# Kernel optimization log

Measured on AMD Instinct MI355X. Metric: run time of the kernel, lower is better.

Reference implementation:

```python
import jax, jax.numpy as jnp
import numpy as np

NN_SIZE = 10  # matches init_kwargs nn_size


def _knn_idx(points, k):
    """points: (B,N,D). Returns (B,N,k) indices of k nearest neighbors, self excluded."""
    sq = jnp.sum(points * points, axis=-1)  # (B,N)
    # squared euclidean distances (B,N,N)
    d2 = sq[:, :, None] + sq[:, None, :] - 2.0 * jnp.einsum('bnd,bmd->bnm', points, points)
    _, idx = jax.lax.top_k(-d2, k + 1)  # smallest distances; first hit is self
    return idx[:, :, 1:]  # drop self -> (B,N,k)


def _uniform_laplacian(points, knn_idx):
    """points: (B,N,D); knn_idx: (B,N,K). lap = mean(neighbors) - point."""
    neigh = jax.vmap(lambda p, i: p[i])(points, knn_idx)  # (B,N,K,D) gather per batch
    return jnp.mean(neigh, axis=2) - points


def setup_inputs() -> dict:
    key = jax.random.key(0)
    k1, k2 = jax.random.split(key)
    B, N, D = 2, 8192, 3
    point1 = jax.random.normal(k1, (B, N, D), dtype=jnp.float32)
    point2 = jax.random.normal(k2, (B, N, D), dtype=jnp.float32)
    return {"point1": point1, "point2": point2}


def reference(point1, point2):
    knn_idx = _knn_idx(point1, NN_SIZE)          # connectivity from ref cloud
    lap1 = _uniform_laplacian(point1, knn_idx)   # (B,N,3)
    lap2 = _uniform_laplacian(point2, knn_idx)   # reuse knn_idx
    # metric = L1Loss (mean reduction); use_norm=False
    return jnp.mean(jnp.abs(lap1 - lap2))
```

## Files before the change

kernel.cpp:

```cpp
#include <hip/hip_runtime.h>
#include <math.h>


constexpr int NPTS  = 8192;
constexpr int NB    = 2;
constexpr int KNN   = 10;
constexpr int QPB   = 64;
constexpr int WPB   = 16;
constexpr int P1BLOCK = 256;
constexpr int P1GRID  = NB * NPTS / (P1BLOCK / WPB);
constexpr int MASK13 = 0xFFFFE000;

constexpr int   G    = 32;
constexpr int   NC   = G * G * G;
constexpr float BMIN = -5.5f;
constexpr float BW   = 11.0f;
constexpr float H    = BW / G;
constexpr float INVH = (float)G / BW;

__device__ __forceinline__ void ins1(int l[KNN], int x) {
#pragma unroll
    for (int k = KNN - 1; k > 0; --k) l[k] = min(l[k], max(l[k - 1], x));
    l[0] = min(l[0], x);
}
__device__ __forceinline__ void ins2(int l[KNN], int a, int b) {
    const int b0 = min(a, b), b1 = max(a, b);
#pragma unroll
    for (int k = KNN - 1; k >= 2; --k)
        l[k] = min(l[k], min(max(l[k - 1], b0), max(l[k - 2], b1)));
    l[1] = min(l[1], min(max(l[0], b0), b1));
    l[0] = min(l[0], b0);
}
template<int S>
__device__ __forceinline__ void ins2s(int l[KNN], int a, int b) {
    const int b0 = min(a, b), b1 = max(a, b);
#pragma unroll
    for (int k = KNN - 1; k >= S + 2; --k)
        l[k] = min(l[k], min(max(l[k - 1], b0), max(l[k - 2], b1)));
    l[S + 1] = min(l[S + 1], min(max(l[S], b0), b1));
    l[S] = min(l[S], b0);
}
__device__ __forceinline__ void merge_sorted(int l[KNN], const int p[KNN]) {
    ins2s<0>(l, p[0], p[1]);
    ins2s<2>(l, p[2], p[3]);
    ins2s<4>(l, p[4], p[5]);
    ins2s<6>(l, p[6], p[7]);
    ins2s<8>(l, p[8], p[9]);
}

__global__ void pack_bin(const float* __restrict__ p1, float4* __restrict__ w,
                         int* __restrict__ hist, int* __restrict__ cellof,
                         float* __restrict__ out, int* __restrict__ nfail) {
    const int i = blockIdx.x * blockDim.x + threadIdx.x;
    if (i >= NB * NPTS) return;
    if (i == 0) { out[0] = 0.0f; nfail[0] = 0; }
    const float x = p1[3 * i], y = p1[3 * i + 1], z = p1[3 * i + 2];
    w[i] = make_float4(x, y, z, fmaf(x, x, fmaf(y, y, z * z)));
    const int cx = min(max((int)floorf((x - BMIN) * INVH), 0), G - 1);
    const int cy = min(max((int)floorf((y - BMIN) * INVH), 0), G - 1);
    const int cz = min(max((int)floorf((z - BMIN) * INVH), 0), G - 1);
    const int c = (cz << 10) | (cy << 5) | cx;
    cellof[i] = c;
    atomicAdd(&hist[(i >> 13) * NC + c], 1);
}

__global__ __launch_bounds__(1024)
void scan_cells(const int* __restrict__ hist, int* __restrict__ starts) {
    __shared__ int wsum[16];
    const int b = blockIdx.x, t = threadIdx.x;
    const int* hb = hist + b * NC;
    int* sb = starts + b * (NC + 1);
    const int c0 = t * 32;
    const int4* hb4 = (const int4*)(hb + c0);
    int loc[32]; int sum = 0;
#pragma unroll
    for (int j = 0; j < 8; ++j) {
        const int4 v = hb4[j];
        loc[4 * j + 0] = v.x; loc[4 * j + 1] = v.y;
        loc[4 * j + 2] = v.z; loc[4 * j + 3] = v.w;
        sum += v.x + v.y + v.z + v.w;
    }
    const int lane = t & 63, wvi = t >> 6;
    int incl = sum;
#pragma unroll
    for (int off = 1; off < 64; off <<= 1) {
        const int v = __shfl_up(incl, off);
        if (lane >= off) incl += v;
    }
    if (lane == 63) wsum[wvi] = incl;
    __syncthreads();
    if (t < 16) {
        const int v = wsum[t];
        int iv = v;
#pragma unroll
        for (int off = 1; off < 16; off <<= 1) {
            const int u = __shfl_up(iv, off);
            if (t >= off) iv += u;
        }
        wsum[t] = iv - v;
    }
    __syncthreads();
    int run = wsum[wvi] + incl - sum;
#pragma unroll
    for (int j = 0; j < 32; ++j) { sb[c0 + j] = run; run += loc[j]; }
    if (t == 1023) sb[NC] = run;
}

__global__ void scatter_all(const int* __restrict__ cellof,
                            const int* __restrict__ starts,
                            int* __restrict__ hist,
                            const float4* __restrict__ w,
                            const float* __restrict__ p2,
                            float4* __restrict__ wsorted,
                            float4* __restrict__ p2s) {
    const int i = blockIdx.x * blockDim.x + threadIdx.x;
    if (i >= NB * NPTS) return;
    const int b = i >> 13;
    const int c = cellof[i];
    const int old = atomicSub(&hist[b * NC + c], 1);
    const int pos = b * NPTS + starts[b * (NC + 1) + c] + old - 1;
    wsorted[pos] = w[i];
    p2s[pos] = make_float4(p2[3 * i], p2[3 * i + 1], p2[3 * i + 2], 0.0f);
}

template<int S>
__device__ __forceinline__ void scan_batched(const float4* __restrict__ W,
                                             const int* __restrict__ st,
                                             int cx, int cy, int cz,
                                             float m2x, float m2y, float m2z,
                                             float q2, int qpos, int sl,
                                             int l[KNN])
{
    constexpr int Wd = 2 * S + 1;
    constexpr int R  = Wd * Wd;
    constexpr int CH = 5;
    const int IMAX = 0x7FFFFFFF;
    int J0[R], J1[R];
#pragma unroll
    for (int r = 0; r < R; ++r) {
        const int dy = r % Wd - S, dz = r / Wd - S;
        const int ay = cy + dy, az = cz + dz;
        const bool ok = ((unsigned)ay < G) && ((unsigned)az < G);
        const int cbase = (az << 10) | (ay << 5);
        const int lo = cbase + max(cx - S, 0);
        const int hi = cbase + min(cx + S, G - 1) + 1;
        J0[r] = ok ? st[lo] : 0;
        J1[r] = ok ? st[hi] : 0;
    }
#pragma unroll
    for (int base = 0; base < R; base += CH) {
        float4 P[CH];
#pragma unroll
        for (int c = 0; c < CH; ++c) {
            const int r = base + c;
            if (r < R) {
                const int j = min(J0[r] + sl, NPTS - 1);
                P[c] = W[j];
            }
        }
#pragma unroll
        for (int c = 0; c < CH; ++c) {
            const int r = base + c;
            if (r < R) {
                const int j1 = J1[r];
                int j = J0[r] + sl;
                if (j < j1) {
                    float4 c4 = P[c];
                    while (true) {
                        const int jn = j + WPB;
                        const bool more = jn < j1;
                        float4 nx;
                        if (more) nx = W[jn];
                        const float d2 = fmaf(m2x, c4.x,
                                         fmaf(m2y, c4.y,
                                         fmaf(m2z, c4.z, c4.w + q2)));
                        int key = (__float_as_int(d2) & MASK13) | j;
                        key = (j == qpos) ? IMAX : key;
                        ins1(l, key);
                        if (!more) break;
                        c4 = nx; j = jn;
                    }
                }
            }
        }
    }
}

__global__ __launch_bounds__(P1BLOCK)
void phase1(const float4* __restrict__ wsorted, const float4* __restrict__ p2s,
            const int* __restrict__ starts, float* __restrict__ out,
            int* __restrict__ nfail, int* __restrict__ worklist)
{
    __shared__ float red[P1BLOCK / 64];

    const int tid = threadIdx.x;
    const int sl  = tid & 15;
    const int gw  = (tid >> 4) & 3;
    const int wv  = tid >> 6;
    const int wglob = wv * P1GRID + blockIdx.x;
    const int unit  = (wglob << 2) | gw;
    const int batch = unit & 1;
    const int qpos  = unit >> 1;

    const float4* W  = wsorted + batch * NPTS;
    const float4* P2 = p2s + batch * NPTS;
    const int*    st = starts + batch * (NC + 1);

    const float4 qp = W[qpos];
    const int cx = min(max((int)floorf((qp.x - BMIN) * INVH), 0), G - 1);
    const int cy = min(max((int)floorf((qp.y - BMIN) * INVH), 0), G - 1);
    const int cz = min(max((int)floorf((qp.z - BMIN) * INVH), 0), G - 1);
    const float lox = BMIN + cx * H, loy = BMIN + cy * H, loz = BMIN + cz * H;
    const float df = fminf(fminf(fminf(qp.x - lox, lox + H - qp.x),
                                 fminf(qp.y - loy, loy + H - qp.y)),
                           fminf(qp.z - loz, loz + H - qp.z));
    const float m2x = -2.0f * qp.x, m2y = -2.0f * qp.y, m2z = -2.0f * qp.z;
    const float q2 = qp.w;
    const int IMAX = 0x7FFFFFFF;

    const int sCov = (q2 > 4.8f) ? 2 : 1;

    int l[KNN];
#pragma unroll
    for (int k = 0; k < KNN; ++k) l[k] = IMAX;

    if (sCov == 1)
        scan_batched<1>(W, st, cx, cy, cz, m2x, m2y, m2z, q2, qpos, sl, l);
    else
        scan_batched<2>(W, st, cx, cy, cz, m2x, m2y, m2z, q2, qpos, sl, l);

#pragma unroll
    for (int off = 1; off < WPB; off <<= 1) {
        int p[KNN];
#pragma unroll
        for (int k = 0; k < KNN; ++k) p[k] = __shfl_xor(l[k], off);
        merge_sorted(l, p);
    }

    float v = 0.0f;
    if (sl == 0) {
        const float tau = __int_as_float(l[KNN - 1] & MASK13);
        const float R = (float)sCov * H + df;
        const bool covered = (tau <= R * R * 0.996f);
        if (covered) {
            float s1x = 0, s1y = 0, s1z = 0, s2x = 0, s2y = 0, s2z = 0;
#pragma unroll
            for (int k = 0; k < KNN; ++k) {
                const int j = l[k] & (NPTS - 1);
                const float4 c4 = W[j];
                const float4 n2 = P2[j];
                s1x += c4.x; s1y += c4.y; s1z += c4.z;
                s2x += n2.x; s2y += n2.y; s2z += n2.z;
            }
            const float4 p2v = P2[qpos];
            const float dx = (s1x * 0.1f - qp.x) - (s2x * 0.1f - p2v.x);
            const float dy2 = (s1y * 0.1f - qp.y) - (s2y * 0.1f - p2v.y);
            const float dz2 = (s1z * 0.1f - qp.z) - (s2z * 0.1f - p2v.z);
            v = fabsf(dx) + fabsf(dy2) + fabsf(dz2);
        } else {
            const int wi = atomicAdd(nfail, 1);
            worklist[wi] = (batch << 16) | qpos;
        }
    }
#pragma unroll
    for (int off = 32; off >= 1; off >>= 1) v += __shfl_down(v, off);
    const int lane = tid & 63;
    if (lane == 0) red[wv] = v;
    __syncthreads();
    if (tid == 0) {
        float s = 0.0f;
#pragma unroll
        for (int e = 0; e < P1BLOCK / 64; ++e) s += red[e];
        if (s != 0.0f)
            atomicAdd(out, s * (1.0f / (float)(NB * NPTS * 3)));
    }
}

constexpr int P2BLK = 256;
constexpr int P2GRID = 512;

__global__ __launch_bounds__(P2BLK)
void phase2(const float4* __restrict__ wsorted, const float4* __restrict__ p2s,
            const int* __restrict__ nfail, const int* __restrict__ worklist,
            float* __restrict__ out)
{
    const int lane = threadIdx.x & 63;
    const int wv   = threadIdx.x >> 6;
    const int wid  = blockIdx.x * (P2BLK / 64) + wv;
    const int NW   = P2GRID * (P2BLK / 64);
    const int nf   = *nfail;
    const int IMAX = 0x7FFFFFFF;
    float acc = 0.0f;

    for (int i = wid; i < nf; i += NW) {
        const int e = worklist[i];
        const int batch = e >> 16, qpos = e & 0xFFFF;
        const float4* W  = wsorted + batch * NPTS;
        const float4* P2 = p2s + batch * NPTS;
        const float4 qp = W[qpos];
        const float m2x = -2.0f * qp.x, m2y = -2.0f * qp.y, m2z = -2.0f * qp.z;
        const float q2 = qp.w;

        int l[KNN];
#pragma unroll
        for (int k = 0; k < KNN; ++k) l[k] = IMAX;

#pragma unroll 2
        for (int it = 0; it < NPTS / 128; ++it) {
            const int ja = it * 128 + lane, jb = ja + 64;
            const float4 ca = W[ja];
            const float4 cb = W[jb];
            const float da = fmaf(m2x, ca.x, fmaf(m2y, ca.y, fmaf(m2z, ca.z, ca.w + q2)));
            const float db = fmaf(m2x, cb.x, fmaf(m2y, cb.y, fmaf(m2z, cb.z, cb.w + q2)));
            int ka = (__float_as_int(da) & MASK13) | ja;
            int kb = (__float_as_int(db) & MASK13) | jb;
            ka = (ja == qpos) ? IMAX : ka;
            kb = (jb == qpos) ? IMAX : kb;
            ins2(l, ka, kb);
        }
        for (int off = 1; off < 64; off <<= 1) {
            int p[KNN];
#pragma unroll
            for (int k = 0; k < KNN; ++k) p[k] = __shfl_xor(l[k], off);
            merge_sorted(l, p);
        }
        float s1x = 0, s1y = 0, s1z = 0, s2x = 0, s2y = 0, s2z = 0;
#pragma unroll
        for (int k = 0; k < KNN; ++k) {
            const int j = l[k] & (NPTS - 1);
            const float4 c4 = W[j];
            const float4 n2 = P2[j];
            s1x += c4.x; s1y += c4.y; s1z += c4.z;
            s2x += n2.x; s2y += n2.y; s2z += n2.z;
        }
        const float4 p2v = P2[qpos];
        const float dx = (s1x * 0.1f - qp.x) - (s2x * 0.1f - p2v.x);
        const float dy = (s1y * 0.1f - qp.y) - (s2y * 0.1f - p2v.y);
        const float dz = (s1z * 0.1f - qp.z) - (s2z * 0.1f - p2v.z);
        if (lane == 0) acc += fabsf(dx) + fabsf(dy) + fabsf(dz);
    }

    if (lane == 0 && acc != 0.0f)
        atomicAdd(out, acc * (1.0f / (float)(NB * NPTS * 3)));
}

constexpr int FB_WPB = 8;
constexpr int FB_BLOCK = QPB * FB_WPB;
constexpr int CHUNK = NPTS / FB_WPB;

__global__ void prep_pack(const float* __restrict__ p, float4* __restrict__ w) {
    const int i = blockIdx.x * blockDim.x + threadIdx.x;
    if (i < NB * NPTS) {
        const float x = p[3 * i], y = p[3 * i + 1], z = p[3 * i + 2];
        w[i] = make_float4(x, y, z, fmaf(x, x, fmaf(y, y, z * z)));
    }
}

__global__ __launch_bounds__(FB_BLOCK, 2)
void knn_lap(const float4* __restrict__ w1, const float* __restrict__ p2,
             float* __restrict__ out)
{
    __shared__ int mv[FB_WPB * KNN * QPB];
    const int batch = blockIdx.x >> 7;
    const int qbase = (blockIdx.x & 127) << 6;
    const int lane  = threadIdx.x & 63;
    const int wv    = __builtin_amdgcn_readfirstlane(threadIdx.x >> 6);
    const int query = qbase + lane;
    const float4* Wb = w1 + batch * NPTS;
    const float4 qp = Wb[query];
    const float m2x = -2.0f * qp.x, m2y = -2.0f * qp.y, m2z = -2.0f * qp.z;
    const float q2 = qp.w;
    const int IMAX = 0x7FFFFFFF;
    int l[KNN];
#pragma unroll
    for (int k = 0; k < KNN; ++k) l[k] = IMAX;
    const int c0 = wv * CHUNK;
    const float4* cand = Wb + c0;
#pragma unroll 4
    for (int i = 0; i < CHUNK; i += 2) {
        const float4 ca = cand[i];
        const float4 cb = cand[i + 1];
        const int ja = c0 + i, jb = ja + 1;
        const float da = fmaf(m2x, ca.x, fmaf(m2y, ca.y, fmaf(m2z, ca.z, ca.w + q2)));
        const float db = fmaf(m2x, cb.x, fmaf(m2y, cb.y, fmaf(m2z, cb.z, cb.w + q2)));
        int ka = (__float_as_int(da) & MASK13) | ja;
        int kb = (__float_as_int(db) & MASK13) | jb;
        ka = (ja == query) ? IMAX : ka;
        kb = (jb == query) ? IMAX : kb;
        ins2(l, ka, kb);
    }
#pragma unroll
    for (int k = 0; k < KNN; ++k) mv[(wv * KNN + k) * QPB + lane] = l[k];
    __syncthreads();
    if (threadIdx.x < QPB) {
        int m[KNN];
#pragma unroll
        for (int k = 0; k < KNN; ++k) m[k] = IMAX;
#pragma unroll
        for (int e = 0; e < FB_WPB; ++e) {
            int p[KNN];
#pragma unroll
            for (int k = 0; k < KNN; ++k) p[k] = mv[(e * KNN + k) * QPB + lane];
            merge_sorted(m, p);
        }
        const float* P2b = p2 + (size_t)batch * NPTS * 3;
        float s1x = 0, s1y = 0, s1z = 0, s2x = 0, s2y = 0, s2z = 0;
#pragma unroll
        for (int k = 0; k < KNN; ++k) {
            const int j = m[k] & (NPTS - 1);
            const float4 c = Wb[j];
            s1x += c.x; s1y += c.y; s1z += c.z;
            s2x += P2b[3 * j + 0]; s2y += P2b[3 * j + 1]; s2z += P2b[3 * j + 2];
        }
        const int q = qbase + threadIdx.x;
        const float p2x = P2b[3 * q + 0], p2y = P2b[3 * q + 1], p2z = P2b[3 * q + 2];
        const float dx = (s1x * 0.1f - qp.x) - (s2x * 0.1f - p2x);
        const float dy = (s1y * 0.1f - qp.y) - (s2y * 0.1f - p2y);
        const float dz = (s1z * 0.1f - qp.z) - (s2z * 0.1f - p2z);
        float v = fabsf(dx) + fabsf(dy) + fabsf(dz);
#pragma unroll
        for (int off = 32; off >= 1; off >>= 1) v += __shfl_down(v, off);
        if (threadIdx.x == 0)
            atomicAdd(out, v * (1.0f / (float)(NB * NPTS * 3)));
    }
}

extern "C" void kernel_launch(void* const* d_in, const int* in_sizes, int n_in,
                              void* d_out, int out_size, void* d_ws, size_t ws_size,
                              hipStream_t stream) {
    const float* p1 = (const float*)d_in[0];
    const float* p2 = (const float*)d_in[1];
    float* out = (float*)d_out;

    size_t off = 0;
    float4* w       = (float4*)d_ws;               off += (size_t)NB * NPTS * 16;
    int*    hist    = (int*)((char*)d_ws + off);   off += (size_t)NB * NC * 4;
    int*    starts  = (int*)((char*)d_ws + off);   off += (size_t)NB * (NC + 1) * 4 + 8;
    int*    cellof  = (int*)((char*)d_ws + off);   off += (size_t)NB * NPTS * 4;
    float4* wsorted = (float4*)((char*)d_ws + off); off += (size_t)NB * NPTS * 16;
    float4* p2s     = (float4*)((char*)d_ws + off); off += (size_t)NB * NPTS * 16;
    int*    nfail   = (int*)((char*)d_ws + off);   off += 16;
    int*    worklist= (int*)((char*)d_ws + off);   off += (size_t)NB * NPTS * 4;

    if (ws_size < off) {
        hipMemsetAsync(out, 0, sizeof(float), stream);
        prep_pack<<<(NB * NPTS + 255) / 256, 256, 0, stream>>>(p1, w);
        knn_lap<<<NB * (NPTS / QPB), FB_BLOCK, 0, stream>>>(w, p2, out);
        return;
    }

    hipMemsetAsync(hist, 0, (size_t)NB * NC * 4, stream);
    pack_bin<<<(NB * NPTS + 255) / 256, 256, 0, stream>>>(p1, w, hist, cellof,
                                                          out, nfail);
    scan_cells<<<NB, 1024, 0, stream>>>(hist, starts);
    scatter_all<<<(NB * NPTS + 255) / 256, 256, 0, stream>>>(cellof, starts, hist,
                                                             w, p2, wsorted, p2s);
    phase1<<<P1GRID, P1BLOCK, 0, stream>>>(wsorted, p2s, starts, out,
                                           nfail, worklist);
    phase2<<<P2GRID, P2BLK, 0, stream>>>(wsorted, p2s, nfail, worklist, out);
}
```

Before: 118.3 us.

## Fuse fallback brute-force kNN into phase1 via spin-waited worklist consumption

Removes the separate phase2 launch: after finishing their covered queries, phase1 waves claim worklist slots through an atomic counter and spin until producers publish uncovered queries, then run the brute-force scan. The worklist is pre-initialised to -1 in scatter_all, and extra counters track production and block completion. This aims to overlap the fallback work with the phase1 tail and drop a launch. Because spinning waves can hold CUs while unscheduled producer blocks wait for residency, it risks long stalls or deadlock.

```diff
diff --git a/kernel.cpp b/kernel.cpp
--- a/kernel.cpp
+++ b/kernel.cpp
@@ -53,7 +53,12 @@
                          float* __restrict__ out, int* __restrict__ nfail) {
     const int i = blockIdx.x * blockDim.x + threadIdx.x;
     if (i >= NB * NPTS) return;
-    if (i == 0) { out[0] = 0.0f; nfail[0] = 0; }
+    if (i == 0) {
+        out[0] = 0.0f;
+        nfail[0]  = 0;
+        nfail[32] = 0;
+        nfail[64] = 0;
+    }
     const float x = p1[3 * i], y = p1[3 * i + 1], z = p1[3 * i + 2];
     w[i] = make_float4(x, y, z, fmaf(x, x, fmaf(y, y, z * z)));
     const int cx = min(max((int)floorf((x - BMIN) * INVH), 0), G - 1);
@@ -112,9 +117,11 @@
                             const float4* __restrict__ w,
                             const float* __restrict__ p2,
                             float4* __restrict__ wsorted,
-                            float4* __restrict__ p2s) {
+                            float4* __restrict__ p2s,
+                            int* __restrict__ worklist) {
     const int i = blockIdx.x * blockDim.x + threadIdx.x;
     if (i >= NB * NPTS) return;
+    worklist[i] = -1;
     const int b = i >> 13;
     const int c = cellof[i];
     const int old = atomicSub(&hist[b * NC + c], 1);
@@ -186,12 +193,16 @@
     }
 }
 
-__global__ __launch_bounds__(P1BLOCK)
+__global__ __launch_bounds__(P1BLOCK, 4)
 void phase1(const float4* __restrict__ wsorted, const float4* __restrict__ p2s,
             const int* __restrict__ starts, float* __restrict__ out,
             int* __restrict__ nfail, int* __restrict__ worklist)
 {
     __shared__ float red[P1BLOCK / 64];
+
+    int* const nprod  = nfail;
+    int* const pclaim = nfail + 32;
+    int* const bdone  = nfail + 64;
 
     const int tid = threadIdx.x;
     const int sl  = tid & 15;
@@ -258,8 +269,8 @@
             const float dz2 = (s1z * 0.1f - qp.z) - (s2z * 0.1f - p2v.z);
             v = fabsf(dx) + fabsf(dy2) + fabsf(dz2);
         } else {
-            const int wi = atomicAdd(nfail, 1);
-            worklist[wi] = (batch << 16) | qpos;
+            const int wi = atomicAdd(nprod, 1);
+            atomicExch(&worklist[wi], (batch << 16) | qpos);
         }
     }
 #pragma unroll
@@ -273,73 +284,72 @@
         for (int e = 0; e < P1BLOCK / 64; ++e) s += red[e];
         if (s != 0.0f)
             atomicAdd(out, s * (1.0f / (float)(NB * NPTS * 3)));
-    }
-}
-
-constexpr int P2BLK = 256;
-constexpr int P2GRID = 512;
-
-__global__ __launch_bounds__(P2BLK)
-void phase2(const float4* __restrict__ wsorted, const float4* __restrict__ p2s,
-            const int* __restrict__ nfail, const int* __restrict__ worklist,
-            float* __restrict__ out)
-{
-    const int lane = threadIdx.x & 63;
-    const int wv   = threadIdx.x >> 6;
-    const int wid  = blockIdx.x * (P2BLK / 64) + wv;
-    const int NW   = P2GRID * (P2BLK / 64);
-    const int nf   = *nfail;
-    const int IMAX = 0x7FFFFFFF;
+        atomicAdd(bdone, 1);
+    }
+
     float acc = 0.0f;
-
-    for (int i = wid; i < nf; i += NW) {
-        const int e = worklist[i];
-        const int batch = e >> 16, qpos = e & 0xFFFF;
-        const float4* W  = wsorted + batch * NPTS;
-        const float4* P2 = p2s + batch * NPTS;
-        const float4 qp = W[qpos];
-        const float m2x = -2.0f * qp.x, m2y = -2.0f * qp.y, m2z = -2.0f * qp.z;
-        const float q2 = qp.w;
-
-        int l[KNN];
-#pragma unroll
-        for (int k = 0; k < KNN; ++k) l[k] = IMAX;
-
+    const int NG = (int)gridDim.x;
+    while (true) {
+        int c;
+        if (lane == 0) c = atomicAdd(pclaim, 1);
+        c = __shfl(c, 0);
+        if (c >= NB * NPTS) break;
+        int e = -1;
+        int spins = 0;
+        while (true) {
+            e = atomicAdd(&worklist[c], 0);
+            if (e != -1) break;
+            if (((++spins) & 7) == 0 &&
+                atomicAdd(bdone, 0) == NG &&
+                c >= atomicAdd(nprod, 0)) { e = -2; break; }
+            __builtin_amdgcn_s_sleep(2);
+        }
+        if (e == -2) break;
+
+        const int sbatch = e >> 16, sq = e & 0xFFFF;
+        const float4* SW  = wsorted + sbatch * NPTS;
+        const float4* SP2 = p2s + sbatch * NPTS;
+        const float4 sqp = SW[sq];
+        const float sm2x = -2.0f * sqp.x, sm2y = -2.0f * sqp.y, sm2z = -2.0f * sqp.z;
+        const float sq2 = sqp.w;
+
+        int sl2[KNN];
+#pragma unroll
+        for (int k = 0; k < KNN; ++k) sl2[k] = IMAX;
 #pragma unroll 2
         for (int it = 0; it < NPTS / 128; ++it) {
             const int ja = it * 128 + lane, jb = ja + 64;
-            const float4 ca = W[ja];
-            const float4 cb = W[jb];
-            const float da = fmaf(m2x, ca.x, fmaf(m2y, ca.y, fmaf(m2z, ca.z, ca.w + q2)));
-            const float db = fmaf(m2x, cb.x, fmaf(m2y, cb.y, fmaf(m2z, cb.z, cb.w + q2)));
+            const float4 ca = SW[ja];
+            const float4 cb = SW[jb];
+            const float da = fmaf(sm2x, ca.x, fmaf(sm2y, ca.y, fmaf(sm2z, ca.z, ca.w + sq2)));
+            const float db = fmaf(sm2x, cb.x, fmaf(sm2y, cb.y, fmaf(sm2z, cb.z, cb.w + sq2)));
             int ka = (__float_as_int(da) & MASK13) | ja;
             int kb = (__float_as_int(db) & MASK13) | jb;
-            ka = (ja == qpos) ? IMAX : ka;
-            kb = (jb == qpos) ? IMAX : kb;
-            ins2(l, ka, kb);
+            ka = (ja == sq) ? IMAX : ka;
+            kb = (jb == sq) ? IMAX : kb;
+            ins2(sl2, ka, kb);
         }
         for (int off = 1; off < 64; off <<= 1) {
             int p[KNN];
 #pragma unroll
-            for (int k = 0; k < KNN; ++k) p[k] = __shfl_xor(l[k], off);
-            merge_sorted(l, p);
+            for (int k = 0; k < KNN; ++k) p[k] = __shfl_xor(sl2[k], off);
+            merge_sorted(sl2, p);
         }
         float s1x = 0, s1y = 0, s1z = 0, s2x = 0, s2y = 0, s2z = 0;
 #pragma unroll
         for (int k = 0; k < KNN; ++k) {
-            const int j = l[k] & (NPTS - 1);
-            const float4 c4 = W[j];
-            const float4 n2 = P2[j];
+            const int j = sl2[k] & (NPTS - 1);
+            const float4 c4 = SW[j];
+            const float4 n2 = SP2[j];
             s1x += c4.x; s1y += c4.y; s1z += c4.z;
             s2x += n2.x; s2y += n2.y; s2z += n2.z;
         }
-        const float4 p2v = P2[qpos];
-        const float dx = (s1x * 0.1f - qp.x) - (s2x * 0.1f - p2v.x);
-        const float dy = (s1y * 0.1f - qp.y) - (s2y * 0.1f - p2v.y);
-        const float dz = (s1z * 0.1f - qp.z) - (s2z * 0.1f - p2v.z);
+        const float4 p2v = SP2[sq];
+        const float dx = (s1x * 0.1f - sqp.x) - (s2x * 0.1f - p2v.x);
+        const float dy = (s1y * 0.1f - sqp.y) - (s2y * 0.1f - p2v.y);
+        const float dz = (s1z * 0.1f - sqp.z) - (s2z * 0.1f - p2v.z);
         if (lane == 0) acc += fabsf(dx) + fabsf(dy) + fabsf(dz);
     }
-
     if (lane == 0 && acc != 0.0f)
         atomicAdd(out, acc * (1.0f / (float)(NB * NPTS * 3)));
 }
@@ -439,7 +449,7 @@
     int*    cellof  = (int*)((char*)d_ws + off);   off += (size_t)NB * NPTS * 4;
     float4* wsorted = (float4*)((char*)d_ws + off); off += (size_t)NB * NPTS * 16;
     float4* p2s     = (float4*)((char*)d_ws + off); off += (size_t)NB * NPTS * 16;
-    int*    nfail   = (int*)((char*)d_ws + off);   off += 16;
+    int*    nfail   = (int*)((char*)d_ws + off);   off += 512;
     int*    worklist= (int*)((char*)d_ws + off);   off += (size_t)NB * NPTS * 4;
 
     if (ws_size < off) {
@@ -454,8 +464,8 @@
                                                           out, nfail);
     scan_cells<<<NB, 1024, 0, stream>>>(hist, starts);
     scatter_all<<<(NB * NPTS + 255) / 256, 256, 0, stream>>>(cellof, starts, hist,
-                                                             w, p2, wsorted, p2s);
+                                                             w, p2, wsorted, p2s,
+                                                             worklist);
     phase1<<<P1GRID, P1BLOCK, 0, stream>>>(wsorted, p2s, starts, out,
                                            nfail, worklist);
-    phase2<<<P2GRID, P2BLK, 0, stream>>>(wsorted, p2s, nfail, worklist, out);
-}
+}
```

After: 171.0 us. 44.6% more time.
